# Kernel tuning notes

Measured on AMD Instinct MI355X. Metric: run time of the kernel, lower is better.

Reference implementation:

```python
import jax, jax.numpy as jnp
import numpy as np

B, S, D = 2, 2048, 2048
NH, NKV, HD = 32, 8, 64
RATIO = NH // NKV  # 4
EPS = 1e-6


def setup_inputs() -> dict:
    key = jax.random.key(0)
    ks = jax.random.split(key, 6)
    x = jax.random.normal(ks[0], (B, S, D), dtype=jnp.float32)
    # weights stored (in, out) so projection is x @ W
    wq = jax.random.normal(ks[1], (D, NH * HD), dtype=jnp.float32) * 0.02
    wk = jax.random.normal(ks[2], (D, NKV * HD), dtype=jnp.float32) * 0.02
    wv = jax.random.normal(ks[3], (D, NKV * HD), dtype=jnp.float32) * 0.02
    wo = jax.random.normal(ks[4], (NH * HD, D), dtype=jnp.float32) * 0.02
    q_scale = jnp.ones((HD,), dtype=jnp.float32)
    k_scale = jnp.ones((HD,), dtype=jnp.float32)
    # RoPE tables (S, HD): duplicated-half layout
    inv_freq = 1.0 / (10000.0 ** (np.arange(0, HD, 2, dtype=np.float32) / HD))
    t = np.arange(S, dtype=np.float32)
    freqs = np.outer(t, inv_freq)  # (S, HD/2)
    emb = np.concatenate([freqs, freqs], axis=-1)  # (S, HD)
    cos = jnp.asarray(np.cos(emb))
    sin = jnp.asarray(np.sin(emb))
    # causal mask: True above diagonal = masked
    mask = jnp.triu(jnp.ones((S, S), dtype=jnp.bool_), k=1)
    return {"x": x, "wq": wq, "wk": wk, "wv": wv, "wo": wo,
            "q_scale": q_scale, "k_scale": k_scale,
            "cos": cos, "sin": sin, "mask": mask}


def _rms_norm(x, scale):
    # Qwen3-compatible: compute in fp32, cast back
    idt = x.dtype
    xf = x.astype(jnp.float32)
    nx = xf * jax.lax.rsqrt(jnp.mean(xf * xf, axis=-1, keepdims=True) + EPS)
    return (nx * scale).astype(idt)


def _rope(x, cos, sin):
    # x: (b, h, s, hd); cos/sin: (s, hd)
    hd = x.shape[-1]
    x1, x2 = x[..., : hd // 2], x[..., hd // 2:]
    rot = jnp.concatenate([-x2, x1], axis=-1)
    return x * cos[None, None] + rot * sin[None, None]


def reference(x, wq, wk, wv, wo, q_scale, k_scale, cos, sin, mask):
    b, sl, _ = x.shape
    q = (x @ wq).reshape(b, sl, NH, HD).transpose(0, 2, 1, 3)    # (b, nh, s, hd)
    k = (x @ wk).reshape(b, sl, NKV, HD).transpose(0, 2, 1, 3)   # (b, nkv, s, hd)
    v = (x @ wv).reshape(b, sl, NKV, HD).transpose(0, 2, 1, 3)   # (b, nkv, s, hd)
    q = _rms_norm(q, q_scale)
    k = _rms_norm(k, k_scale)
    q = _rope(q, cos, sin)
    k = _rope(k, cos, sin)
    # GQA: repeat KV heads
    k = jnp.repeat(k, RATIO, axis=1)  # (b, nh, s, hd)
    v = jnp.repeat(v, RATIO, axis=1)
    scores = jnp.einsum('bhqd,bhkd->bhqk', q, k) / jnp.sqrt(jnp.float32(HD))
    scores = jnp.where(mask[None, None], jnp.finfo(scores.dtype).min, scores)
    attn = jax.nn.softmax(scores, axis=-1)
    out = jnp.einsum('bhqk,bhkd->bhqd', attn, v)
    out = out.transpose(0, 2, 1, 3).reshape(b, sl, NH * HD)
    return out @ wo
```

## Files before the change

### kernel.cpp

```cpp
#include <hip/hip_runtime.h>
#include <hip/hip_bf16.h>

typedef float f32x4 __attribute__((ext_vector_type(4)));
typedef float f32x16 __attribute__((ext_vector_type(16)));
typedef short s16x8 __attribute__((ext_vector_type(8)));
typedef unsigned short u16;
typedef unsigned short u16x8 __attribute__((ext_vector_type(8)));
typedef unsigned short u16x4 __attribute__((ext_vector_type(4)));
typedef unsigned int u32;
typedef unsigned int u32x4 __attribute__((ext_vector_type(4)));

#define MROWS 4096
#define NQKV  3072
#define DMODEL 2048

#define EXP2(x) __builtin_amdgcn_exp2f(x)

__device__ __forceinline__ u16 f2bf(float f) {
  __hip_bfloat16 h = __float2bfloat16(f);
  return __builtin_bit_cast(u16, h);
}
__device__ __forceinline__ float bf2f(u16 u) {
  __hip_bfloat16 h = __builtin_bit_cast(__hip_bfloat16, u);
  return __bfloat162float(h);
}

__device__ __forceinline__ u32 cvtpk(float a, float b) {
  u32 r;
  asm("v_cvt_pk_bf16_f32 %0, %1, %2" : "=v"(r) : "v"(a), "v"(b));
  return r;
}

typedef __attribute__((address_space(3))) unsigned int lds_u32_t;
typedef const __attribute__((address_space(1))) unsigned int glb_u32_t;
__device__ __forceinline__ void gload_lds16(const void* g, void* l) {
  __builtin_amdgcn_global_load_lds((glb_u32_t*)g, (lds_u32_t*)l, 16, 0, 0);
}

__global__ __launch_bounds__(256) void k_conv_x(const float* __restrict__ x, u16* __restrict__ o) {
  size_t i = ((size_t)blockIdx.x * 256 + threadIdx.x) * 4;
  float4 v = *(const float4*)(x + i);
  u16x4 r = { f2bf(v.x), f2bf(v.y), f2bf(v.z), f2bf(v.w) };
  *(u16x4*)(o + i) = r;
}

__global__ __launch_bounds__(256) void k_transw(const float* __restrict__ src, u16* __restrict__ dst,
                                                int N, int K) {
  __shared__ u16 t[64][68];
  int n0 = blockIdx.x * 64, k0 = blockIdx.y * 64;
  int tid = threadIdx.x;
#pragma unroll
  for (int r = 0; r < 4; ++r) {
    int k = r * 16 + (tid >> 4);
    int n = (tid & 15) * 4;
    float4 v = *(const float4*)(src + (size_t)(k0 + k) * N + n0 + n);
    t[n + 0][k] = f2bf(v.x);
    t[n + 1][k] = f2bf(v.y);
    t[n + 2][k] = f2bf(v.z);
    t[n + 3][k] = f2bf(v.w);
  }
  __syncthreads();
#pragma unroll
  for (int r = 0; r < 4; ++r) {
    int n = r * 16 + (tid >> 4);
    int k = (tid & 15) * 4;
    u16x4 o = { t[n][k], t[n][k + 1], t[n][k + 2], t[n][k + 3] };
    *(u16x4*)(dst + (size_t)(n0 + n) * K + k0 + k) = o;
  }
}

template <int BM, int BN, typename OutT>
__global__ __launch_bounds__(512, 2)
void k_gemm8(const u16* __restrict__ A, const u16* __restrict__ Bt,
             OutT* __restrict__ C, int M, int N, int K, int nbx) {
  static_assert(BM == 128, "A staging assumes one full 512x16B round");
  constexpr int WM = 2, WN = 4;
  constexpr int MF = BM / 16 / WM;
  constexpr int NF = BN / 16 / WN;
  __shared__ u16 sA[2][2][BM][32];
  __shared__ u16 sB[2][2][BN][32];
  const int nwg = gridDim.x;
  const int chunk = nwg >> 3;
  const int wg = (blockIdx.x & 7) * chunk + (blockIdx.x >> 3);
  const int m0 = (wg / nbx) * BM, n0 = (wg % nbx) * BN;
  const int tid = threadIdx.x;
  const int l = tid & 63;
  const int lo = l & 15, hi = l >> 4;
  const int wid = tid >> 6;
  const int wm = wid >> 2, wn = wid & 3;
  const int nkt = K >> 6;

  f32x4 acc[MF][NF] = {};

  auto STAGE = [&](int buf, int ks, int t) {
    {
      const int D = tid * 16;
      const int row = D >> 6;
      const int srcb = (D & 63) ^ (((row >> 1) & 3) << 4);
      gload_lds16((const char*)(A + (size_t)(m0 + row) * K + t * 64 + ks * 32) + srcb,
                  (char*)(&sA[buf][ks][0][0]) + D);
    }
#pragma unroll
    for (int i = 0; i < 2; ++i) {
      const int u = i * 512 + tid;
      if (u < BN * 4) {
        const int D = u * 16;
        const int row = D >> 6;
        const int srcb = (D & 63) ^ (((row >> 1) & 3) << 4);
        gload_lds16((const char*)(Bt + (size_t)(n0 + row) * K + t * 64 + ks * 32) + srcb,
                    (char*)(&sB[buf][ks][0][0]) + D);
      }
    }
  };

  auto WAITVM = [&]() {
    if constexpr (BN == 192) {
      if (wid < 4) asm volatile("s_waitcnt vmcnt(3)" ::: "memory");
      else         asm volatile("s_waitcnt vmcnt(2)" ::: "memory");
    } else if constexpr (BN == 256) {
      asm volatile("s_waitcnt vmcnt(3)" ::: "memory");
    } else {
      asm volatile("s_waitcnt vmcnt(2)" ::: "memory");
    }
  };

  auto PHASE = [&](int buf, int ks, int t1, bool st, int vmmode) {
    s16x8 a[MF], b[NF];
#pragma unroll
    for (int mf = 0; mf < MF; ++mf) {
      const int row = wm * (MF * 16) + mf * 16 + lo;
      a[mf] = *(const s16x8*)((const char*)(&sA[buf][ks][0][0]) + row * 64 +
                              ((hi * 16) ^ (((row >> 1) & 3) << 4)));
    }
#pragma unroll
    for (int nf = 0; nf < NF; ++nf) {
      const int row = wn * (NF * 16) + nf * 16 + lo;
      b[nf] = *(const s16x8*)((const char*)(&sB[buf][ks][0][0]) + row * 64 +
                              ((hi * 16) ^ (((row >> 1) & 3) << 4)));
    }
    if (st) STAGE(buf ^ 1, ks, t1);
    __builtin_amdgcn_sched_barrier(0);
    __builtin_amdgcn_s_barrier();
    asm volatile("s_waitcnt lgkmcnt(0)" ::: "memory");
    __builtin_amdgcn_sched_barrier(0);
    __builtin_amdgcn_s_setprio(1);
#pragma unroll
    for (int mf = 0; mf < MF; ++mf)
#pragma unroll
      for (int nf = 0; nf < NF; ++nf)
        acc[mf][nf] = __builtin_amdgcn_mfma_f32_16x16x32_bf16(a[mf], b[nf], acc[mf][nf], 0, 0, 0);
    __builtin_amdgcn_s_setprio(0);
    if (vmmode == 1) WAITVM();
    else if (vmmode == 2) asm volatile("s_waitcnt vmcnt(0)" ::: "memory");
    __builtin_amdgcn_sched_barrier(0);
    __builtin_amdgcn_s_barrier();
  };

  STAGE(0, 0, 0);
  STAGE(0, 1, 0);
  WAITVM();
  __builtin_amdgcn_s_barrier();

  for (int t = 0; t < nkt; ++t) {
    const int buf = t & 1;
    const bool st = (t + 1 < nkt);
    PHASE(buf, 0, t + 1, st, st ? 1 : 2);
    PHASE(buf, 1, t + 1, st, st ? 1 : 0);
  }

#pragma unroll
  for (int mf = 0; mf < MF; ++mf)
#pragma unroll
    for (int nf = 0; nf < NF; ++nf)
#pragma unroll
      for (int r = 0; r < 4; ++r) {
        const int row = m0 + wm * (MF * 16) + mf * 16 + hi * 4 + r;
        const int col = n0 + wn * (NF * 16) + nf * 16 + lo;
        if constexpr (__is_same(OutT, float)) C[(size_t)row * N + col] = acc[mf][nf][r];
        else                                  C[(size_t)row * N + col] = f2bf(acc[mf][nf][r]);
      }
}

__global__ __launch_bounds__(256) void k_normrope(const u16* __restrict__ qkv, u16* __restrict__ qn,
                                                  u16* __restrict__ kn, const float* __restrict__ qs,
                                                  const float* __restrict__ ksc,
                                                  const float* __restrict__ cosb,
                                                  const float* __restrict__ sinb) {
  int j = blockIdx.x * 4 + (threadIdx.x >> 6);
  int l = threadIdx.x & 63;
  bool isQ = j < MROWS * 32;
  int m, head, incol;
  if (isQ) { m = j >> 5; head = j & 31; incol = head * 64; }
  else     { int j2 = j - MROWS * 32; m = j2 >> 3; head = j2 & 7; incol = 2048 + head * 64; }
  float v = bf2f(qkv[(size_t)m * NQKV + incol + l]);
  float ss = v * v;
#pragma unroll
  for (int off = 1; off < 64; off <<= 1) ss += __shfl_xor(ss, off, 64);
  float inv = rsqrtf(ss * (1.0f / 64.0f) + 1e-6f);
  float nx = v * inv * (isQ ? qs[l] : ksc[l]);
  int s = m & 2047;
  float c = cosb[s * 64 + l], sn = sinb[s * 64 + l];
  float partner = __shfl_xor(nx, 32, 64);
  float rot = (l < 32) ? -partner : partner;
  float outv = nx * c + rot * sn;
  if (isQ) {
    outv *= 0.125f * 1.44269504088896f;
    qn[(size_t)m * 2048 + incol + l] = f2bf(outv);
  } else {
    kn[(size_t)m * 512 + head * 64 + l] = f2bf(outv);
  }
}

__global__ __launch_bounds__(256) void k_vtrans(const u16* __restrict__ qkv, u16* __restrict__ vt) {
  __shared__ u16 t[64][68];
  int s0 = blockIdx.x * 64;
  int bk = blockIdx.y;
  int tid = threadIdx.x;
#pragma unroll
  for (int r = 0; r < 4; ++r) {
    int s = r * 16 + (tid >> 4);
    int d = (tid & 15) * 4;
    u16x4 v = *(const u16x4*)(qkv + (size_t)((bk >> 3) * 2048 + s0 + s) * NQKV + 2560 + (bk & 7) * 64 + d);
    t[d + 0][s] = v[0];
    t[d + 1][s] = v[1];
    t[d + 2][s] = v[2];
    t[d + 3][s] = v[3];
  }
  __syncthreads();
#pragma unroll
  for (int r = 0; r < 4; ++r) {
    int d = r * 16 + (tid >> 4);
    int sl = (tid & 15) * 4;
    u16x4 o = { t[d][sl], t[d][sl + 1], t[d][sl + 2], t[d][sl + 3] };
    *(u16x4*)(vt + (size_t)(bk * 64 + d) * 2048 + s0 + sl) = o;
  }
}

__global__ __launch_bounds__(512, 2) void k_attn(const u16* __restrict__ qn, const u16* __restrict__ kn,
                                                 const u16* __restrict__ vt, u16* __restrict__ aout) {
  __shared__ char sKV[4][2][64 * 128];
  float* mO = (float*)&sKV[0][0][0];
  float* mL = mO + 128 * 65;
  const int bid = blockIdx.x;
  const int kvh = bid & 7;
  const int b = (bid >> 3) & 1;
  const int hsub = (bid >> 4) & 3;
  const int p = bid >> 6;
  const int h = kvh * 4 + hsub;
  const int tid = threadIdx.x, l = tid & 63;
  const int w = tid >> 6, qw = w & 3, half = w >> 2;
  const int l31 = l & 31, l5 = l >> 5;
  const int qtA = 15 - p, qtB = p;
  const u16* kbase = kn + (size_t)(b * 2048) * 512 + kvh * 64;
  const u16* vbase = vt + (size_t)((b * 8 + kvh) * 64) * 2048;
  const int st = tid >> 8;
  const int stid = tid & 255;
  const int srow = stid >> 3;
  const int scol = (stid & 7) * 8;
  const int sg_t = srow >> 4, sg_h = (srow >> 3) & 1, sg_j = srow & 7;
  const int krow0 = 32 * (sg_t >> 1) + 8 * ((sg_t & 1) * 2 + (sg_j >> 2)) + 4 * sg_h + (sg_j & 3);

  u16x8 krg0, krg1, vrg0, vrg1;
  int stbuf = 0;
  auto issue = [&](int baset) {
    const int tile = baset + st;
    const int kv0 = tile * 64;
    stbuf = tile & 3;
    krg0 = *(const u16x8*)(kbase + (size_t)(kv0 + srow) * 512 + scol);
    krg1 = *(const u16x8*)(kbase + (size_t)(kv0 + srow + 32) * 512 + scol);
    vrg0 = *(const u16x8*)(vbase + (size_t)srow * 2048 + kv0 + scol);
    vrg1 = *(const u16x8*)(vbase + (size_t)(srow + 32) * 2048 + kv0 + scol);
  };
  auto stash = [&]() {
    char* sK = sKV[stbuf][0];
    char* sV = sKV[stbuf][1];
    const int cb = scol * 2;
    const int k0_ = krow0, k1_ = krow0 + 32;
    *(u16x8*)(sK + k0_ * 128 + (cb ^ ((k0_ & 7) << 4))) = krg0;
    *(u16x8*)(sK + k1_ * 128 + (cb ^ ((k1_ & 7) << 4))) = krg1;
    const int r0 = srow, r1 = srow + 32;
    *(u16x8*)(sV + r0 * 128 + (cb ^ ((r0 & 7) << 4))) = vrg0;
    *(u16x8*)(sV + r1 * 128 + (cb ^ ((r1 & 7) << 4))) = vrg1;
  };

  s16x8 qf[4];
  f32x16 O0, O1;
  float lst;

  for (int mem = 0; mem < 2; ++mem) {
    const int qt = mem ? qtB : qtA;
    const int row = qw * 32 + l31;
    {
      const u16* qp = qn + (size_t)(b * 2048 + qt * 128 + row) * 2048 + h * 64 + l5 * 8;
#pragma unroll
      for (int ki = 0; ki < 4; ++ki) qf[ki] = *(const s16x8*)(qp + ki * 16);
#pragma unroll
      for (int r = 0; r < 16; ++r) { O0[r] = 0.f; O1[r] = 0.f; }
      lst = 0.f;
    }
    issue(0);
    stash();
    __syncthreads();
    const int nss = qt + 1;
    for (int i = 0; i < nss; ++i) {
      const int T = 2 * i + half;
      const char* sK = sKV[T & 3][0];
      const char* sV = sKV[T & 3][1];
      if (i + 1 < nss) issue(2 * i + 2);
      f32x16 sc0, sc1;
#pragma unroll
      for (int r = 0; r < 16; ++r) { sc0[r] = 0.f; sc1[r] = 0.f; }
      __builtin_amdgcn_s_setprio(1);
#pragma unroll
      for (int ki = 0; ki < 4; ++ki) {
        const int cb = ki * 32 + l5 * 16;
        const int r0 = l31, r1 = 32 + l31;
        s16x8 a0 = *(const s16x8*)(sK + r0 * 128 + (cb ^ ((r0 & 7) << 4)));
        s16x8 a1 = *(const s16x8*)(sK + r1 * 128 + (cb ^ ((r1 & 7) << 4)));
        sc0 = __builtin_amdgcn_mfma_f32_32x32x16_bf16(a0, qf[ki], sc0, 0, 0, 0);
        sc1 = __builtin_amdgcn_mfma_f32_32x32x16_bf16(a1, qf[ki], sc1, 0, 0, 0);
      }
      __builtin_amdgcn_s_setprio(0);
      if (T >= 2 * qt) {
        const int qrow = qt * 128 + row;
        const int kb0 = T * 64 + 8 * l5;
#pragma unroll
        for (int r = 0; r < 16; ++r) {
          const int klocal = 16 * (r >> 3) + 4 * ((r >> 2) & 1) + (r & 3);
          if (kb0 + klocal > qrow) sc0[r] = -1e30f;
          if (kb0 + 32 + klocal > qrow) sc1[r] = -1e30f;
        }
      }
      float rs = 0.f;
      u32 pk0[4][2], pk1[4][2];
#pragma unroll
      for (int g = 0; g < 4; ++g) {
        float a0 = EXP2(sc0[4*g+0]), a1 = EXP2(sc0[4*g+1]);
        float a2 = EXP2(sc0[4*g+2]), a3 = EXP2(sc0[4*g+3]);
        float b0 = EXP2(sc1[4*g+0]), b1 = EXP2(sc1[4*g+1]);
        float b2 = EXP2(sc1[4*g+2]), b3 = EXP2(sc1[4*g+3]);
        rs += ((a0 + a1) + (a2 + a3)) + ((b0 + b1) + (b2 + b3));
        pk0[g][0] = cvtpk(a0, a1);
        pk0[g][1] = cvtpk(a2, a3);
        pk1[g][0] = cvtpk(b0, b1);
        pk1[g][1] = cvtpk(b2, b3);
      }
      rs += __shfl_xor(rs, 32, 64);
      lst += rs;
#define PV_STEP(PK, GB, KB)                                                   \
      {                                                                       \
        u32x4 wv_ = { PK[GB][0], PK[GB][1], PK[GB+1][0], PK[GB+1][1] };       \
        s16x8 pb = __builtin_bit_cast(s16x8, wv_);                            \
        const int cb = (KB) * 32 + l5 * 16;                                   \
        const int rv0 = l31, rv1 = 32 + l31;                                  \
        s16x8 v0 = *(const s16x8*)(sV + rv0 * 128 + (cb ^ ((rv0 & 7) << 4))); \
        s16x8 v1 = *(const s16x8*)(sV + rv1 * 128 + (cb ^ ((rv1 & 7) << 4))); \
        __builtin_amdgcn_s_setprio(1);                                        \
        O0 = __builtin_amdgcn_mfma_f32_32x32x16_bf16(v0, pb, O0, 0, 0, 0);    \
        O1 = __builtin_amdgcn_mfma_f32_32x32x16_bf16(v1, pb, O1, 0, 0, 0);    \
        __builtin_amdgcn_s_setprio(0);                                        \
      }
      PV_STEP(pk0, 0, 0)
      PV_STEP(pk0, 2, 1)
      PV_STEP(pk1, 0, 2)
      PV_STEP(pk1, 2, 3)
#undef PV_STEP
      if (i + 1 < nss) stash();
      __syncthreads();
    }
    if (half == 1) {
#pragma unroll
      for (int g = 0; g < 4; ++g)
#pragma unroll
        for (int j = 0; j < 4; ++j) {
          const int d = 8 * g + 4 * l5 + j;
          mO[row * 65 + d] = O0[4*g+j];
          mO[row * 65 + 32 + d] = O1[4*g+j];
        }
      if (l5 == 0) mL[row] = lst;
    }
    __syncthreads();
    if (half == 0) {
      const float inv = 1.0f / (lst + mL[row]);
      const size_t rowoff = (size_t)(b * 2048 + qt * 128 + row) * 2048 + h * 64;
#pragma unroll
      for (int g = 0; g < 4; ++g) {
        const int d0 = 8 * g + 4 * l5;
        u16x4 o0 = { f2bf((O0[4*g+0] + mO[row*65+d0+0]) * inv),
                     f2bf((O0[4*g+1] + mO[row*65+d0+1]) * inv),
                     f2bf((O0[4*g+2] + mO[row*65+d0+2]) * inv),
                     f2bf((O0[4*g+3] + mO[row*65+d0+3]) * inv) };
        *(u16x4*)(aout + rowoff + d0) = o0;
        u16x4 o1 = { f2bf((O1[4*g+0] + mO[row*65+32+d0+0]) * inv),
                     f2bf((O1[4*g+1] + mO[row*65+32+d0+1]) * inv),
                     f2bf((O1[4*g+2] + mO[row*65+32+d0+2]) * inv),
                     f2bf((O1[4*g+3] + mO[row*65+32+d0+3]) * inv) };
        *(u16x4*)(aout + rowoff + 32 + d0) = o1;
      }
    }
    __syncthreads();
  }
}

extern "C" void kernel_launch(void* const* d_in, const int* in_sizes, int n_in,
                              void* d_out, int out_size, void* d_ws, size_t ws_size,
                              hipStream_t stream) {
  (void)in_sizes; (void)n_in; (void)out_size; (void)ws_size;
  const float* x    = (const float*)d_in[0];
  const float* wq   = (const float*)d_in[1];
  const float* wk   = (const float*)d_in[2];
  const float* wv   = (const float*)d_in[3];
  const float* wo   = (const float*)d_in[4];
  const float* qs   = (const float*)d_in[5];
  const float* ksc  = (const float*)d_in[6];
  const float* cosb = (const float*)d_in[7];
  const float* sinb = (const float*)d_in[8];
  float* out = (float*)d_out;
  char* ws = (char*)d_ws;
  u16* xbf   = (u16*)(ws);
  u16* wqkvt = (u16*)(ws + 16777216);
  u16* wot   = (u16*)(ws + 29360128);
  u16* qkv   = (u16*)(ws + 37748736);
  u16* qn    = (u16*)(ws + 62914560);
  u16* kn    = (u16*)(ws + 79691776);
  u16* vt    = (u16*)(ws + 83886080);
  u16* aout  = (u16*)(ws + 88080384);

  k_conv_x<<<8192, 256, 0, stream>>>(x, xbf);
  k_transw<<<dim3(32, 32), 256, 0, stream>>>(wq, wqkvt, 2048, 2048);
  k_transw<<<dim3(8, 32), 256, 0, stream>>>(wk, wqkvt + (size_t)2048 * 2048, 512, 2048);
  k_transw<<<dim3(8, 32), 256, 0, stream>>>(wv, wqkvt + (size_t)2560 * 2048, 512, 2048);
  k_transw<<<dim3(32, 32), 256, 0, stream>>>(wo, wot, 2048, 2048);
  k_gemm8<128, 192, u16><<<512, 512, 0, stream>>>(xbf, wqkvt, qkv, MROWS, NQKV, 2048, 16);
  k_normrope<<<40960, 256, 0, stream>>>(qkv, qn, kn, qs, ksc, cosb, sinb);
  k_vtrans<<<dim3(32, 16), 256, 0, stream>>>(qkv, vt);
  k_attn<<<512, 512, 0, stream>>>(qn, kn, vt, aout);
  k_gemm8<128, 128, float><<<512, 512, 0, stream>>>(aout, wot, out, MROWS, DMODEL, 2048, 16);
}
```

Before: 207.1 us.

## Load K/V fragments directly from global memory instead of LDS staging

Removes the LDS double/quad-buffered K/V staging pipeline and per-iteration block barriers in the attention kernel. Each wave now reads its K and V MFMA operands straight from global memory (relying on L1/L2 caching), and shared memory is used only for the final cross-half reduction. This cuts barrier and LDS traffic but makes every wave issue its own global loads, losing reuse across the four query waves and exposing memory latency without explicit prefetch.

```diff
diff --git a/kernel.cpp b/kernel.cpp
--- a/kernel.cpp
+++ b/kernel.cpp
@@ -238,9 +238,9 @@
 
 __global__ __launch_bounds__(512, 2) void k_attn(const u16* __restrict__ qn, const u16* __restrict__ kn,
                                                  const u16* __restrict__ vt, u16* __restrict__ aout) {
-  __shared__ char sKV[4][2][64 * 128];
-  float* mO = (float*)&sKV[0][0][0];
-  float* mL = mO + 128 * 65;
+  __shared__ float mOL[128 * 65 + 128];
+  float* mO = mOL;
+  float* mL = mOL + 128 * 65;
   const int bid = blockIdx.x;
   const int kvh = bid & 7;
   const int b = (bid >> 3) & 1;
@@ -253,35 +253,8 @@
   const int qtA = 15 - p, qtB = p;
   const u16* kbase = kn + (size_t)(b * 2048) * 512 + kvh * 64;
   const u16* vbase = vt + (size_t)((b * 8 + kvh) * 64) * 2048;
-  const int st = tid >> 8;
-  const int stid = tid & 255;
-  const int srow = stid >> 3;
-  const int scol = (stid & 7) * 8;
-  const int sg_t = srow >> 4, sg_h = (srow >> 3) & 1, sg_j = srow & 7;
-  const int krow0 = 32 * (sg_t >> 1) + 8 * ((sg_t & 1) * 2 + (sg_j >> 2)) + 4 * sg_h + (sg_j & 3);
-
-  u16x8 krg0, krg1, vrg0, vrg1;
-  int stbuf = 0;
-  auto issue = [&](int baset) {
-    const int tile = baset + st;
-    const int kv0 = tile * 64;
-    stbuf = tile & 3;
-    krg0 = *(const u16x8*)(kbase + (size_t)(kv0 + srow) * 512 + scol);
-    krg1 = *(const u16x8*)(kbase + (size_t)(kv0 + srow + 32) * 512 + scol);
-    vrg0 = *(const u16x8*)(vbase + (size_t)srow * 2048 + kv0 + scol);
-    vrg1 = *(const u16x8*)(vbase + (size_t)(srow + 32) * 2048 + kv0 + scol);
-  };
-  auto stash = [&]() {
-    char* sK = sKV[stbuf][0];
-    char* sV = sKV[stbuf][1];
-    const int cb = scol * 2;
-    const int k0_ = krow0, k1_ = krow0 + 32;
-    *(u16x8*)(sK + k0_ * 128 + (cb ^ ((k0_ & 7) << 4))) = krg0;
-    *(u16x8*)(sK + k1_ * 128 + (cb ^ ((k1_ & 7) << 4))) = krg1;
-    const int r0 = srow, r1 = srow + 32;
-    *(u16x8*)(sV + r0 * 128 + (cb ^ ((r0 & 7) << 4))) = vrg0;
-    *(u16x8*)(sV + r1 * 128 + (cb ^ ((r1 & 7) << 4))) = vrg1;
-  };
+  const int B_ = (l31 >> 3) & 3, h_ = (l31 >> 2) & 1, c_ = l31 & 3;
+  const int sigi = 16 * (B_ >> 1) + 8 * h_ + 4 * (B_ & 1) + c_;
 
   s16x8 qf[4];
   f32x16 O0, O1;
@@ -298,25 +271,19 @@
       for (int r = 0; r < 16; ++r) { O0[r] = 0.f; O1[r] = 0.f; }
       lst = 0.f;
     }
-    issue(0);
-    stash();
-    __syncthreads();
     const int nss = qt + 1;
     for (int i = 0; i < nss; ++i) {
       const int T = 2 * i + half;
-      const char* sK = sKV[T & 3][0];
-      const char* sV = sKV[T & 3][1];
-      if (i + 1 < nss) issue(2 * i + 2);
+      const int kv0 = T * 64;
       f32x16 sc0, sc1;
 #pragma unroll
       for (int r = 0; r < 16; ++r) { sc0[r] = 0.f; sc1[r] = 0.f; }
       __builtin_amdgcn_s_setprio(1);
 #pragma unroll
       for (int ki = 0; ki < 4; ++ki) {
-        const int cb = ki * 32 + l5 * 16;
-        const int r0 = l31, r1 = 32 + l31;
-        s16x8 a0 = *(const s16x8*)(sK + r0 * 128 + (cb ^ ((r0 & 7) << 4)));
-        s16x8 a1 = *(const s16x8*)(sK + r1 * 128 + (cb ^ ((r1 & 7) << 4)));
+        const u16* kp = kbase + (size_t)(kv0 + sigi) * 512 + ki * 16 + l5 * 8;
+        s16x8 a0 = *(const s16x8*)kp;
+        s16x8 a1 = *(const s16x8*)(kp + (size_t)32 * 512);
         sc0 = __builtin_amdgcn_mfma_f32_32x32x16_bf16(a0, qf[ki], sc0, 0, 0, 0);
         sc1 = __builtin_amdgcn_mfma_f32_32x32x16_bf16(a1, qf[ki], sc1, 0, 0, 0);
       }
@@ -351,10 +318,9 @@
       {                                                                       \
         u32x4 wv_ = { PK[GB][0], PK[GB][1], PK[GB+1][0], PK[GB+1][1] };       \
         s16x8 pb = __builtin_bit_cast(s16x8, wv_);                            \
-        const int cb = (KB) * 32 + l5 * 16;                                   \
-        const int rv0 = l31, rv1 = 32 + l31;                                  \
-        s16x8 v0 = *(const s16x8*)(sV + rv0 * 128 + (cb ^ ((rv0 & 7) << 4))); \
-        s16x8 v1 = *(const s16x8*)(sV + rv1 * 128 + (cb ^ ((rv1 & 7) << 4))); \
+        const u16* vp = vbase + (size_t)l31 * 2048 + kv0 + (KB) * 16 + l5 * 8; \
+        s16x8 v0 = *(const s16x8*)vp;                                         \
+        s16x8 v1 = *(const s16x8*)(vp + (size_t)32 * 2048);                   \
         __builtin_amdgcn_s_setprio(1);                                        \
         O0 = __builtin_amdgcn_mfma_f32_32x32x16_bf16(v0, pb, O0, 0, 0, 0);    \
         O1 = __builtin_amdgcn_mfma_f32_32x32x16_bf16(v1, pb, O1, 0, 0, 0);    \
@@ -365,9 +331,8 @@
       PV_STEP(pk1, 0, 2)
       PV_STEP(pk1, 2, 3)
 #undef PV_STEP
-      if (i + 1 < nss) stash();
-      __syncthreads();
-    }
+    }
+    __syncthreads();
     if (half == 1) {
 #pragma unroll
       for (int g = 0; g < 4; ++g)
```

New measurement: 281.8 us. 1.36x slower.
